# Performance work log

Measured on AMD Instinct MI355X. Metric: run time of the kernel, lower is better.

## Reference

```python
import jax, jax.numpy as jnp
import numpy as np

VOCAB, DM, H, DH, FF, NL = 50265, 768, 12, 64, 3072, 12
WIN = 256  # one-sided window (attention_window=512)
B, S = 1, 4096


def layer_norm(x, s, b, eps=1e-5):
    mu = x.mean(-1, keepdims=True)
    var = x.var(-1, keepdims=True)
    return (x - mu) * jax.lax.rsqrt(var + eps) * s + b


def sliding_attn(x, key_mask, wq, wk, wv, bq, bk, bv):
    Bb, Ss, _ = x.shape
    nb = Ss // WIN
    q = ((x @ wq + bq) / np.float32(np.sqrt(DH))).reshape(Bb, nb, WIN, H, DH)
    k = (x @ wk + bk).reshape(Bb, Ss, H, DH)
    v = (x @ wv + bv).reshape(Bb, Ss, H, DH)
    pad = [(0, 0), (WIN, WIN), (0, 0), (0, 0)]
    kp = jnp.pad(k, pad).reshape(Bb, nb + 2, WIN, H, DH)
    vp = jnp.pad(v, pad).reshape(Bb, nb + 2, WIN, H, DH)
    mp = jnp.pad(key_mask, [(0, 0), (WIN, WIN)]).reshape(Bb, nb + 2, WIN)
    kwin = jnp.concatenate([kp[:, i:i + nb] for i in range(3)], axis=2)  # [B,nb,3W,H,DH]
    vwin = jnp.concatenate([vp[:, i:i + nb] for i in range(3)], axis=2)
    mwin = jnp.concatenate([mp[:, i:i + nb] for i in range(3)], axis=2)  # [B,nb,3W]
    scores = jnp.einsum('bnqhd,bnkhd->bhnqk', q, kwin)  # [B,H,nb,W,3W]
    rel = jnp.arange(3 * WIN)[None, :] - jnp.arange(WIN)[:, None]
    band = (rel >= 0) & (rel <= 2 * WIN)
    valid = band[None, None, None] & (mwin > 0)[:, None, :, None, :]
    probs = jax.nn.softmax(jnp.where(valid, scores, -1e9), axis=-1)
    out = jnp.einsum('bhnqk,bnkhd->bnqhd', probs, vwin)
    return out.reshape(Bb, Ss, H * DH)


def encode(tokens, mask, word_emb, pos_emb, emb_ln_s, emb_ln_b, qkv_w, qkv_b,
           attn_out_w, attn_out_b, attn_ln_s, attn_ln_b,
           ffn_w1, ffn_b1, ffn_w2, ffn_b2, ffn_ln_s, ffn_ln_b):
    Ss = tokens.shape[1]
    x = word_emb[tokens] + pos_emb[2:2 + Ss][None]  # roberta-style position offset
    x = layer_norm(x, emb_ln_s, emb_ln_b)
    for l in range(NL):
        a = sliding_attn(x, mask, qkv_w[l, 0], qkv_w[l, 1], qkv_w[l, 2],
                         qkv_b[l, 0], qkv_b[l, 1], qkv_b[l, 2])
        x = layer_norm(x + a @ attn_out_w[l] + attn_out_b[l], attn_ln_s[l], attn_ln_b[l])
        h = jax.nn.gelu(x @ ffn_w1[l] + ffn_b1[l], approximate=False)
        x = layer_norm(x + h @ ffn_w2[l] + ffn_b2[l], ffn_ln_s[l], ffn_ln_b[l])
    return x


def setup_inputs() -> dict:
    key = jax.random.key(0)
    ks = iter(jax.random.split(key, 40))
    tokens = jax.random.randint(next(ks), (B, 1, S), 0, VOCAB)
    mask = jnp.ones((B, 1, S), dtype=jnp.int64 if False else jnp.int32)
    essay_tokens = jnp.concatenate([tokens, mask.astype(tokens.dtype)], axis=1)
    g = lambda shape: (jax.random.normal(next(ks), shape, jnp.float32) * 0.02)
    return {
        'essay_tokens': essay_tokens,
        'word_emb': g((VOCAB, DM)), 'pos_emb': g((4098, DM)),
        'emb_ln_s': jnp.ones((DM,)), 'emb_ln_b': jnp.zeros((DM,)),
        'qkv_w': g((NL, 3, DM, DM)), 'qkv_b': g((NL, 3, DM)),
        'attn_out_w': g((NL, DM, DM)), 'attn_out_b': g((NL, DM)),
        'attn_ln_s': jnp.ones((NL, DM)), 'attn_ln_b': jnp.zeros((NL, DM)),
        'ffn_w1': g((NL, DM, FF)), 'ffn_b1': g((NL, FF)),
        'ffn_w2': g((NL, FF, DM)), 'ffn_b2': g((NL, DM)),
        'ffn_ln_s': jnp.ones((NL, DM)), 'ffn_ln_b': jnp.zeros((NL, DM)),
        'cls_w1': g((DM, 512)), 'cls_b1': jnp.zeros((512,)),
        'cls_w2': g((512, 512)), 'cls_b2': jnp.zeros((512,)),
        'cls_w3': g((512, 512)), 'cls_b3': jnp.zeros((512,)),
        'cls_w4': g((512, 2)), 'cls_b4': jnp.zeros((2,)),
    }


def reference(essay_tokens, word_emb, pos_emb, emb_ln_s, emb_ln_b, qkv_w, qkv_b,
              attn_out_w, attn_out_b, attn_ln_s, attn_ln_b,
              ffn_w1, ffn_b1, ffn_w2, ffn_b2, ffn_ln_s, ffn_ln_b,
              cls_w1, cls_b1, cls_w2, cls_b2, cls_w3, cls_b3, cls_w4, cls_b4):
    tokens = essay_tokens[:, 0, :].astype(jnp.int32)
    mask = essay_tokens[:, 1, :].astype(jnp.int32)
    enc = encode(tokens, mask, word_emb, pos_emb, emb_ln_s, emb_ln_b, qkv_w, qkv_b,
                 attn_out_w, attn_out_b, attn_ln_s, attn_ln_b,
                 ffn_w1, ffn_b1, ffn_w2, ffn_b2, ffn_ln_s, ffn_ln_b)
    # torch.no_grad() on the transformer
    enc = jax.lax.stop_gradient(enc)
    h = enc @ cls_w1 + cls_b1
    h = h @ cls_w2 + cls_b2
    h = h @ cls_w3 + cls_b3
    logits = h @ cls_w4 + cls_b4  # [B,S,2]
    out = logits[..., 0]          # chunk(..., 2, dim=-1)[0] then flatten(1)
    return out.reshape(out.shape[0], -1)
```

## Files before the change

### kernel.cpp

```cpp
#include <hip/hip_runtime.h>
#include <cmath>

#define S_LEN 4096
#define DMODEL 768
#define NHEAD 12
#define DHEAD 64
#define FFDIM 3072
#define NLAYER 12
#define WINR 256

typedef float f32x4 __attribute__((ext_vector_type(4)));
typedef short s8v __attribute__((ext_vector_type(8)));
typedef __bf16 b8v __attribute__((ext_vector_type(8)));

__device__ __forceinline__ short f2b(float f) {
  unsigned u = __builtin_bit_cast(unsigned, f);
  unsigned r = (u + 0x7fffu + ((u >> 16) & 1u)) >> 16;
  return (short)r;
}
__device__ __forceinline__ float b2f(short s) {
  unsigned u = ((unsigned)(unsigned short)s) << 16;
  return __builtin_bit_cast(float, u);
}
__device__ __forceinline__ f32x4 mfma16(s8v a, s8v b, f32x4 c) {
  return __builtin_amdgcn_mfma_f32_16x16x32_bf16(
      __builtin_bit_cast(b8v, a), __builtin_bit_cast(b8v, b), c, 0, 0, 0);
}
__device__ __forceinline__ void gl_lds16(const short* g, short* l) {
  __builtin_amdgcn_global_load_lds(
      (const __attribute__((address_space(1))) unsigned int*)g,
      (__attribute__((address_space(3))) unsigned int*)l, 16, 0, 0);
}

#define QSCALE 0.18033688011112042f
#define THR2 11.5415603f

__device__ __forceinline__ void wtr_tile(const float* __restrict__ src,
                                         short* __restrict__ dst, int K, int N,
                                         int k0, int n0, int t,
                                         short (*tile)[65]) {
  {
    int kr = t >> 2, nc = (t & 3) * 16;
    const float* p = src + (long)(k0 + kr) * N + n0 + nc;
#pragma unroll
    for (int q = 0; q < 4; ++q) {
      float4 f = *(const float4*)(p + q * 4);
      tile[kr][nc + q * 4 + 0] = f2b(f.x);
      tile[kr][nc + q * 4 + 1] = f2b(f.y);
      tile[kr][nc + q * 4 + 2] = f2b(f.z);
      tile[kr][nc + q * 4 + 3] = f2b(f.w);
    }
  }
  __syncthreads();
  {
    int nr = t >> 2, cc = (t & 3) * 16;
    short* q = dst + (long)(n0 + nr) * K + k0 + cc;
    s8v v0, v1;
#pragma unroll
    for (int j = 0; j < 8; ++j) v0[j] = tile[cc + j][nr];
#pragma unroll
    for (int j = 0; j < 8; ++j) v1[j] = tile[cc + 8 + j][nr];
    *(s8v*)q = v0;
    *(s8v*)(q + 8) = v1;
  }
}

__global__ __launch_bounds__(256) void wtr_kernel(const float* __restrict__ src,
                                                  short* __restrict__ dst,
                                                  int K, int N) {
  __shared__ short tile[64][65];
  wtr_tile(src, dst, K, N, blockIdx.y * 64, blockIdx.x * 64, threadIdx.x, tile);
}

__global__ __launch_bounds__(256) void wtr_layer_kernel(
    const float* __restrict__ qkv, const float* __restrict__ ao,
    const float* __restrict__ w1, const float* __restrict__ w2,
    short* __restrict__ lwq, short* __restrict__ lwa, short* __restrict__ lw1,
    short* __restrict__ lw2) {
  __shared__ short tile[64][65];
  const long DD = (long)DMODEL * DMODEL;
  int id = blockIdx.x;
  const float* src;
  short* dst;
  int K, N, nT, kT;
  if (id < 432) {
    int m = id / 144, r = id % 144;
    src = qkv + m * DD; dst = lwq + m * DD;
    K = DMODEL; N = DMODEL; nT = r % 12; kT = r / 12;
  } else if (id < 576) {
    int r = id - 432;
    src = ao; dst = lwa;
    K = DMODEL; N = DMODEL; nT = r % 12; kT = r / 12;
  } else if (id < 1152) {
    int r = id - 576;
    src = w1; dst = lw1;
    K = DMODEL; N = FFDIM; nT = r % 48; kT = r / 48;
  } else {
    int r = id - 1152;
    src = w2; dst = lw2;
    K = FFDIM; N = DMODEL; nT = r % 12; kT = r / 12;
  }
  wtr_tile(src, dst, K, N, kT * 64, nT * 64, threadIdx.x, tile);
}

template <int EPI, int OUT>
__global__ __launch_bounds__(256, 4) void bgemm_kernel(
    const short* __restrict__ A, const short* __restrict__ Bt,
    const float* __restrict__ bias, void* __restrict__ Cv,
    int N, int K, int Klen, long sB, long sBias, long sC) {
  __shared__ short As[2][128 * 32];
  __shared__ short Bs[2][128 * 32];
  const int t = threadIdx.x, lane = t & 63, w = t >> 6;
  const int lo = lane & 15, hi = lane >> 4;
  const int wm = (w >> 1) * 64, wn = (w & 1) * 64;

  const int gx = gridDim.x;
  const int bid = blockIdx.x + gx * (blockIdx.y + 32 * blockIdx.z);
  const int xcd = bid & 7;
  const int jj_ = bid >> 3;
  const int bx = jj_ % gx;
  const int t2 = jj_ / gx;
  const int by = xcd * 4 + (t2 & 3);
  const int bz = t2 >> 2;

  const long bm = (long)by * 128;
  const int bn = bx * 128;
  Bt += (long)bz * sB;
  const long Koff = (OUT == 2) ? (long)bz * Klen : 0;

  f32x4 acc[4][4];
#pragma unroll
  for (int i = 0; i < 4; ++i)
#pragma unroll
    for (int j = 0; j < 4; ++j) {
      f32x4 zz = {0.f, 0.f, 0.f, 0.f};
      acc[i][j] = zz;
    }

  const int srow = lane >> 2;
  const int schunk = (lane & 3) ^ ((lane >> 3) & 3);
  const short* ga = A + (bm + srow) * (long)K + Koff + schunk * 8;
  const short* gb = Bt + ((long)bn + srow) * K + Koff + schunk * 8;

#define STAGE(buf, koff)                                                   \
  {                                                                        \
    _Pragma("unroll") for (int i = 0; i < 2; ++i) {                        \
      const int r0 = i * 64 + w * 16;                                      \
      gl_lds16(ga + (long)r0 * K + (koff), As[buf] + r0 * 32);             \
      gl_lds16(gb + (long)r0 * K + (koff), Bs[buf] + r0 * 32);             \
    }                                                                      \
  }

  STAGE(0, 0);
  __syncthreads();

  const int nt = Klen >> 5;
  const int rchunk = (hi ^ ((lo >> 1) & 3)) * 8;
  for (int kt = 0; kt < nt; ++kt) {
    const int cur = kt & 1;
    if (kt + 1 < nt) STAGE(cur ^ 1, (kt + 1) * 32);
    s8v af[4], bf[4];
#pragma unroll
    for (int mi = 0; mi < 4; ++mi)
      af[mi] = *(const s8v*)(As[cur] + (wm + mi * 16 + lo) * 32 + rchunk);
#pragma unroll
    for (int ni = 0; ni < 4; ++ni)
      bf[ni] = *(const s8v*)(Bs[cur] + (wn + ni * 16 + lo) * 32 + rchunk);
#pragma unroll
    for (int mi = 0; mi < 4; ++mi)
#pragma unroll
      for (int ni = 0; ni < 4; ++ni)
        acc[mi][ni] = mfma16(af[mi], bf[ni], acc[mi][ni]);
    __syncthreads();
  }
#undef STAGE

  const float sc = (EPI == 2 && bz == 0) ? QSCALE : 1.0f;
  float* Cf = (float*)Cv + (long)bz * sC;
  short* Cs = (short*)Cv + (long)bz * sC;
  const float* bp = bias + (long)bz * sBias;
#pragma unroll
  for (int mi = 0; mi < 4; ++mi)
#pragma unroll
    for (int ni = 0; ni < 4; ++ni) {
      int col = bn + wn + ni * 16 + lo;
      float bb = (OUT == 2) ? 0.f : bp[col];
#pragma unroll
      for (int jj = 0; jj < 4; ++jj) {
        long row = bm + wm + mi * 16 + hi * 4 + jj;
        float v = acc[mi][ni][jj] + bb;
        if (EPI == 2) v *= sc;
        if (EPI == 1) v = 0.5f * v * (1.0f + erff(v * 0.7071067811865476f));
        if (OUT == 1)
          Cs[row * N + col] = f2b(v);
        else
          Cf[row * N + col] = v;
      }
    }
}

__global__ __launch_bounds__(256) void attn_kernel(
    const short* __restrict__ Qb, const short* __restrict__ Kb,
    const short* __restrict__ Vb, const int* __restrict__ maskp,
    short* __restrict__ Ob) {
  __shared__ short Ks[2][64 * 64];
  __shared__ short VT[2][64 * 64];
  __shared__ short Pl[4][16 * 64];

  const int t = threadIdx.x, lane = t & 63, w = t >> 6;
  const int lo = lane & 15, hi = lane >> 4;

  const int bid = blockIdx.x + 64 * blockIdx.y;
  const int xcd = bid & 7, jb = bid >> 3;
  const int qb = xcd * 8 + (jb & 7), h = jb >> 3;

  const int q0 = qb * 64;
  const int qw = q0 + w * 16;
  short* Plw = Pl[w];

  s8v aq[2];
#pragma unroll
  for (int kg = 0; kg < 2; ++kg)
    aq[kg] = *(const s8v*)(Qb + (long)(qw + lo) * DMODEL + h * 64 + kg * 32 +
                           hi * 8);

  f32x4 o[4];
#pragma unroll
  for (int i = 0; i < 4; ++i) {
    f32x4 zz = {0.f, 0.f, 0.f, 0.f};
    o[i] = zz;
  }
  float rm[4], rl[4];
#pragma unroll
  for (int r = 0; r < 4; ++r) { rm[r] = -1e30f; rl[r] = 0.f; }

  const int kstart = max(0, q0 - WINR);
  const int kend = min(S_LEN, q0 + 64 + WINR);
  const int nt = (kend - kstart) >> 6;

  const int krow = lane >> 3;
  const int ksrccol = ((lane & 7) ^ krow) * 8;

  {
#pragma unroll
    for (int i = 0; i < 2; ++i) {
      const int r0 = w * 16 + i * 8;
      gl_lds16(Kb + (long)(kstart + r0 + krow) * DMODEL + h * 64 + ksrccol,
               Ks[0] + r0 * 64);
    }
    const short* pv = Vb + (long)(kstart + lane) * DMODEL + h * 64 + w * 16;
    s8v v0 = *(const s8v*)pv;
    s8v v1 = *(const s8v*)(pv + 8);
#pragma unroll
    for (int j = 0; j < 8; ++j)
      VT[0][(w * 16 + j) * 64 + (lane ^ (j << 3))] = v0[j];
#pragma unroll
    for (int j = 0; j < 8; ++j)
      VT[0][(w * 16 + 8 + j) * 64 + (lane ^ (j << 3))] = v1[j];
  }
  __syncthreads();

  for (int ti = 0; ti < nt; ++ti) {
    const int kt = kstart + ti * 64;
    const int cur = ti & 1;
    const bool pf = (ti + 1 < nt);
    s8v nv0, nv1;
    if (pf) {
#pragma unroll
      for (int i = 0; i < 2; ++i) {
        const int r0 = w * 16 + i * 8;
        gl_lds16(Kb + (long)(kt + 64 + r0 + krow) * DMODEL + h * 64 + ksrccol,
                 Ks[cur ^ 1] + r0 * 64);
      }
      const short* pv = Vb + (long)(kt + 64 + lane) * DMODEL + h * 64 + w * 16;
      nv0 = *(const s8v*)pv;
      nv1 = *(const s8v*)(pv + 8);
    }

    const bool active = (kt + 63 >= qw - WINR) && (kt <= qw + 15 + WINR);
    if (active) {
      f32x4 sacc[4];
#pragma unroll
      for (int i = 0; i < 4; ++i) {
        f32x4 zz = {0.f, 0.f, 0.f, 0.f};
        sacc[i] = zz;
      }
#pragma unroll
      for (int ni = 0; ni < 4; ++ni)
#pragma unroll
        for (int kg = 0; kg < 2; ++kg) {
          const int chunk = (kg * 4 + hi) ^ (lo & 7);
          s8v bk = *(const s8v*)(Ks[cur] + (ni * 16 + lo) * 64 + chunk * 8);
          sacc[ni] = mfma16(aq[kg], bk, sacc[ni]);
        }

      int mval[4];
#pragma unroll
      for (int ni = 0; ni < 4; ++ni) mval[ni] = maskp[kt + ni * 16 + lo];

      float m0[4];
#pragma unroll
      for (int jj = 0; jj < 4; ++jj) {
        const int qg = qw + hi * 4 + jj;
        float mm = -1e30f;
#pragma unroll
        for (int ni = 0; ni < 4; ++ni) {
          int kg = kt + ni * 16 + lo;
          bool val = (kg >= qg - WINR) && (kg <= qg + WINR) && (mval[ni] != 0);
          float sv = val ? sacc[ni][jj] : -1e30f;
          sacc[ni][jj] = sv;
          mm = fmaxf(mm, sv);
        }
        mm = fmaxf(mm, __shfl_xor(mm, 1));
        mm = fmaxf(mm, __shfl_xor(mm, 2));
        mm = fmaxf(mm, __shfl_xor(mm, 4));
        mm = fmaxf(mm, __shfl_xor(mm, 8));
        m0[jj] = mm;
      }

      bool skipf = true;
#pragma unroll
      for (int jj = 0; jj < 4; ++jj) skipf = skipf && (m0[jj] - rm[jj] <= THR2);

      if (__all(skipf)) {
#pragma unroll
        for (int jj = 0; jj < 4; ++jj) {
          float ts = 0.f;
#pragma unroll
          for (int ni = 0; ni < 4; ++ni) {
            float sv = sacc[ni][jj];
            float p = (sv > -1e29f) ? exp2f(sv - rm[jj]) : 0.f;
            sacc[ni][jj] = p;
            ts += p;
          }
          ts += __shfl_xor(ts, 1);
          ts += __shfl_xor(ts, 2);
          ts += __shfl_xor(ts, 4);
          ts += __shfl_xor(ts, 8);
          rl[jj] += ts;
        }
      } else {
#pragma unroll
        for (int jj = 0; jj < 4; ++jj) {
          float mnew = fmaxf(rm[jj], m0[jj]);
          float scl = exp2f(rm[jj] - mnew);
          rm[jj] = mnew;
          float ts = 0.f;
#pragma unroll
          for (int ni = 0; ni < 4; ++ni) {
            float sv = sacc[ni][jj];
            float p = (sv > -1e29f) ? exp2f(sv - mnew) : 0.f;
            sacc[ni][jj] = p;
            ts += p;
          }
          ts += __shfl_xor(ts, 1);
          ts += __shfl_xor(ts, 2);
          ts += __shfl_xor(ts, 4);
          ts += __shfl_xor(ts, 8);
          rl[jj] = rl[jj] * scl + ts;
#pragma unroll
          for (int di = 0; di < 4; ++di) o[di][jj] *= scl;
        }
      }

#pragma unroll
      for (int jj = 0; jj < 4; ++jj) {
        const int qr = hi * 4 + jj;
#pragma unroll
        for (int ni = 0; ni < 4; ++ni) {
          const int chunk = (ni * 2 + (lo >> 3)) ^ (qr & 7);
          Plw[qr * 64 + chunk * 8 + (lo & 7)] = f2b(sacc[ni][jj]);
        }
      }

      s8v ap[2];
#pragma unroll
      for (int kg = 0; kg < 2; ++kg) {
        const int chunk = (kg * 4 + hi) ^ (lo & 7);
        ap[kg] = *(const s8v*)(Plw + lo * 64 + chunk * 8);
      }
#pragma unroll
      for (int di = 0; di < 4; ++di)
#pragma unroll
        for (int kg = 0; kg < 2; ++kg) {
          const int chunk = (kg * 4 + hi) ^ (lo & 7);
          s8v bv = *(const s8v*)(VT[cur] + (di * 16 + lo) * 64 + chunk * 8);
          o[di] = mfma16(ap[kg], bv, o[di]);
        }
    }

    if (pf) {
#pragma unroll
      for (int j = 0; j < 8; ++j)
        VT[cur ^ 1][(w * 16 + j) * 64 + (lane ^ (j << 3))] = nv0[j];
#pragma unroll
      for (int j = 0; j < 8; ++j)
        VT[cur ^ 1][(w * 16 + 8 + j) * 64 + (lane ^ (j << 3))] = nv1[j];
    }
    __syncthreads();
  }

#pragma unroll
  for (int di = 0; di < 4; ++di)
#pragma unroll
    for (int jj = 0; jj < 4; ++jj) {
      long row = qw + hi * 4 + jj;
      Ob[row * DMODEL + h * 64 + di * 16 + lo] = f2b(o[di][jj] / rl[jj]);
    }
}

__global__ __launch_bounds__(256) void embed_ln_kernel(
    const int* __restrict__ tok, const float* __restrict__ wemb,
    const float* __restrict__ pemb, const float* __restrict__ gs,
    const float* __restrict__ gb, float* __restrict__ X,
    short* __restrict__ Xb) {
  __shared__ float sm1[4], sm2[4];
  const int row = blockIdx.x;
  const int tk = tok[row];
  float v[3];
  float s = 0.f, q = 0.f;
#pragma unroll
  for (int i = 0; i < 3; ++i) {
    int c = threadIdx.x + i * 256;
    float x = wemb[(long)tk * DMODEL + c] + pemb[(long)(row + 2) * DMODEL + c];
    v[i] = x;
    s += x;
    q += x * x;
  }
#pragma unroll
  for (int off = 32; off; off >>= 1) {
    s += __shfl_down(s, off);
    q += __shfl_down(q, off);
  }
  int w = threadIdx.x >> 6;
  if ((threadIdx.x & 63) == 0) { sm1[w] = s; sm2[w] = q; }
  __syncthreads();
  s = sm1[0] + sm1[1] + sm1[2] + sm1[3];
  q = sm2[0] + sm2[1] + sm2[2] + sm2[3];
  float mu = s * (1.f / DMODEL);
  float var = q * (1.f / DMODEL) - mu * mu;
  float inv = rsqrtf(var + 1e-5f);
#pragma unroll
  for (int i = 0; i < 3; ++i) {
    int c = threadIdx.x + i * 256;
    float y = (v[i] - mu) * inv * gs[c] + gb[c];
    X[(long)row * DMODEL + c] = y;
    Xb[(long)row * DMODEL + c] = f2b(y);
  }
}

__global__ __launch_bounds__(256) void resln2_kernel(
    float* __restrict__ X, const float* __restrict__ P0,
    const float* __restrict__ P1, const float* __restrict__ bias,
    const float* __restrict__ gs, const float* __restrict__ gb,
    short* __restrict__ Xb) {
  __shared__ float sm1[4], sm2[4];
  const int row = blockIdx.x;
  float v[3];
  float s = 0.f, q = 0.f;
#pragma unroll
  for (int i = 0; i < 3; ++i) {
    int c = threadIdx.x + i * 256;
    long ix = (long)row * DMODEL + c;
    float x = X[ix] + P0[ix] + P1[ix] + bias[c];
    v[i] = x;
    s += x;
    q += x * x;
  }
#pragma unroll
  for (int off = 32; off; off >>= 1) {
    s += __shfl_down(s, off);
    q += __shfl_down(q, off);
  }
  int w = threadIdx.x >> 6;
  if ((threadIdx.x & 63) == 0) { sm1[w] = s; sm2[w] = q; }
  __syncthreads();
  s = sm1[0] + sm1[1] + sm1[2] + sm1[3];
  q = sm2[0] + sm2[1] + sm2[2] + sm2[3];
  float mu = s * (1.f / DMODEL);
  float var = q * (1.f / DMODEL) - mu * mu;
  float inv = rsqrtf(var + 1e-5f);
#pragma unroll
  for (int i = 0; i < 3; ++i) {
    int c = threadIdx.x + i * 256;
    float y = (v[i] - mu) * inv * gs[c] + gb[c];
    X[(long)row * DMODEL + c] = y;
    Xb[(long)row * DMODEL + c] = f2b(y);
  }
}

__global__ __launch_bounds__(256) void cls_final_kernel(
    const short* __restrict__ Hh, const float* __restrict__ w4,
    const float* __restrict__ b4, float* __restrict__ out) {
  const int w = threadIdx.x >> 6, lane = threadIdx.x & 63;
  const int row = blockIdx.x * 4 + w;
  float s = 0.f;
#pragma unroll
  for (int j = 0; j < 8; ++j) {
    int k = lane + j * 64;
    s += b2f(Hh[(long)row * 512 + k]) * w4[k * 2];
  }
#pragma unroll
  for (int off = 32; off; off >>= 1) s += __shfl_down(s, off);
  if (lane == 0) out[row] = s + b4[0];
}

extern "C" void kernel_launch(void* const* d_in, const int* in_sizes, int n_in,
                              void* d_out, int out_size, void* d_ws,
                              size_t ws_size, hipStream_t stream) {
  const int* essay = (const int*)d_in[0];
  const float* wemb = (const float*)d_in[1];
  const float* pemb = (const float*)d_in[2];
  const float* eln_s = (const float*)d_in[3];
  const float* eln_b = (const float*)d_in[4];
  const float* qkv_w = (const float*)d_in[5];
  const float* qkv_b = (const float*)d_in[6];
  const float* aow = (const float*)d_in[7];
  const float* aob = (const float*)d_in[8];
  const float* aln_s = (const float*)d_in[9];
  const float* aln_b = (const float*)d_in[10];
  const float* w1 = (const float*)d_in[11];
  const float* b1 = (const float*)d_in[12];
  const float* w2 = (const float*)d_in[13];
  const float* b2 = (const float*)d_in[14];
  const float* fln_s = (const float*)d_in[15];
  const float* fln_b = (const float*)d_in[16];
  const float* c1w = (const float*)d_in[17];
  const float* c1b = (const float*)d_in[18];
  const float* c2w = (const float*)d_in[19];
  const float* c2b = (const float*)d_in[20];
  const float* c3w = (const float*)d_in[21];
  const float* c3b = (const float*)d_in[22];
  const float* c4w = (const float*)d_in[23];
  const float* c4b = (const float*)d_in[24];

  const long SD = (long)S_LEN * DMODEL;
  const long SF = (long)S_LEN * FFDIM;
  const long SH = (long)S_LEN * 512;
  const long DD = (long)DMODEL * DMODEL;
  const long DF = (long)DMODEL * FFDIM;

  float* X = (float*)d_ws;
  float* P0 = X + SD;
  float* P1 = P0 + SD;
  short* lwq = (short*)(P1 + SD);
  short* lwa = lwq + 3 * DD;
  short* lw1 = lwa + DD;
  short* lw2 = lw1 + DF;
  short* c1T = lw2 + DF;
  short* c2T = c1T + (long)DMODEL * 512;
  short* c3T = c2T + 512L * 512;
  short* Xb = c3T + 512L * 512;
  short* QKVb = Xb + SD;
  short* T1b = QKVb + 3 * SD;
  short* T2b = T1b + SD;
  short* H1 = T2b + SF;
  short* H2 = H1 + SH;
  short* H3 = H2 + SH;
  const long needed = (char*)(H3 + SH) - (char*)d_ws;
  if (ws_size < (size_t)needed) return;

  const int* maskp = essay + S_LEN;

  embed_ln_kernel<<<S_LEN, 256, 0, stream>>>(essay, wemb, pemb, eln_s, eln_b, X,
                                             Xb);

  for (int l = 0; l < NLAYER; ++l) {
    wtr_layer_kernel<<<1728, 256, 0, stream>>>(
        qkv_w + l * 3 * DD, aow + l * DD, w1 + l * DF, w2 + l * DF, lwq, lwa,
        lw1, lw2);

    bgemm_kernel<2, 1><<<dim3(6, 32, 3), 256, 0, stream>>>(
        Xb, lwq, qkv_b + (long)l * 3 * DMODEL, QKVb, DMODEL, DMODEL, DMODEL, DD,
        DMODEL, SD);
    attn_kernel<<<dim3(64, 12), 256, 0, stream>>>(QKVb, QKVb + SD,
                                                  QKVb + 2 * SD, maskp, T1b);
    bgemm_kernel<0, 2><<<dim3(6, 32, 2), 256, 0, stream>>>(
        T1b, lwa, aob, P0, DMODEL, DMODEL, 384, 0, 0, SD);
    resln2_kernel<<<S_LEN, 256, 0, stream>>>(X, P0, P1, aob + (long)l * DMODEL,
                                             aln_s + (long)l * DMODEL,
                                             aln_b + (long)l * DMODEL, Xb);
    bgemm_kernel<1, 1><<<dim3(24, 32, 1), 256, 0, stream>>>(
        Xb, lw1, b1 + (long)l * FFDIM, T2b, FFDIM, DMODEL, DMODEL, 0, 0, 0);
    bgemm_kernel<0, 2><<<dim3(6, 32, 2), 256, 0, stream>>>(
        T2b, lw2, b2, P0, DMODEL, FFDIM, 1536, 0, 0, SD);
    resln2_kernel<<<S_LEN, 256, 0, stream>>>(X, P0, P1, b2 + (long)l * DMODEL,
                                             fln_s + (long)l * DMODEL,
                                             fln_b + (long)l * DMODEL, Xb);
  }

  wtr_kernel<<<dim3(8, 12), 256, 0, stream>>>(c1w, c1T, DMODEL, 512);
  wtr_kernel<<<dim3(8, 8), 256, 0, stream>>>(c2w, c2T, 512, 512);
  wtr_kernel<<<dim3(8, 8), 256, 0, stream>>>(c3w, c3T, 512, 512);

  bgemm_kernel<0, 1><<<dim3(4, 32, 1), 256, 0, stream>>>(
      Xb, c1T, c1b, H1, 512, DMODEL, DMODEL, 0, 0, 0);
  bgemm_kernel<0, 1><<<dim3(4, 32, 1), 256, 0, stream>>>(H1, c2T, c2b, H2, 512,
                                                         512, 512, 0, 0, 0);
  bgemm_kernel<0, 1><<<dim3(4, 32, 1), 256, 0, stream>>>(H2, c3T, c3b, H3, 512,
                                                         512, 512, 0, 0, 0);
  cls_final_kernel<<<S_LEN / 4, 256, 0, stream>>>(H3, c4w, c4b, (float*)d_out);
}
```

Measured before the change: 2.343 ms.

## Pre-transpose V globally, async-stage K/V tiles, store split-K partials in bf16

Adds a separate kernel that transposes V into a head-major [dim, seq] layout, so the attention kernel can stage both K and V tiles with async global-to-LDS loads instead of register loads followed by scattered LDS stores. It also adds a fast masking path for key tiles that lie fully inside the window. The split-K GEMM partial outputs become bf16 instead of fp32, roughly halving the traffic into the residual-layernorm kernel. The costs are an extra kernel launch per layer and lower precision on the partial sums before layernorm.

```diff
diff --git a/kernel.cpp b/kernel.cpp
--- a/kernel.cpp
+++ b/kernel.cpp
@@ -103,6 +103,35 @@
   wtr_tile(src, dst, K, N, kT * 64, nT * 64, threadIdx.x, tile);
 }
 
+__global__ __launch_bounds__(256) void vtr_kernel(const short* __restrict__ Vb,
+                                                  short* __restrict__ VTg) {
+  __shared__ short tile[64][65];
+  const int s0 = blockIdx.x * 64, h = blockIdx.y;
+  const int t = threadIdx.x;
+  {
+    int sr = t >> 2, dc = (t & 3) * 16;
+    const short* p = Vb + (long)(s0 + sr) * DMODEL + h * 64 + dc;
+    s8v a0 = *(const s8v*)p;
+    s8v a1 = *(const s8v*)(p + 8);
+#pragma unroll
+    for (int j = 0; j < 8; ++j) tile[sr][dc + j] = a0[j];
+#pragma unroll
+    for (int j = 0; j < 8; ++j) tile[sr][dc + 8 + j] = a1[j];
+  }
+  __syncthreads();
+  {
+    int dr = t >> 2, sc = (t & 3) * 16;
+    short* q = VTg + (long)(h * 64 + dr) * S_LEN + s0 + sc;
+    s8v v0, v1;
+#pragma unroll
+    for (int j = 0; j < 8; ++j) v0[j] = tile[sc + j][dr];
+#pragma unroll
+    for (int j = 0; j < 8; ++j) v1[j] = tile[sc + 8 + j][dr];
+    *(s8v*)q = v0;
+    *(s8v*)(q + 8) = v1;
+  }
+}
+
 template <int EPI, int OUT>
 __global__ __launch_bounds__(256, 4) void bgemm_kernel(
     const short* __restrict__ A, const short* __restrict__ Bt,
@@ -191,17 +220,17 @@
         float v = acc[mi][ni][jj] + bb;
         if (EPI == 2) v *= sc;
         if (EPI == 1) v = 0.5f * v * (1.0f + erff(v * 0.7071067811865476f));
-        if (OUT == 1)
+        if (OUT == 0)
+          Cf[row * N + col] = v;
+        else
           Cs[row * N + col] = f2b(v);
-        else
-          Cf[row * N + col] = v;
       }
     }
 }
 
 __global__ __launch_bounds__(256) void attn_kernel(
     const short* __restrict__ Qb, const short* __restrict__ Kb,
-    const short* __restrict__ Vb, const int* __restrict__ maskp,
+    const short* __restrict__ VTg, const int* __restrict__ maskp,
     short* __restrict__ Ob) {
   __shared__ short Ks[2][64 * 64];
   __shared__ short VT[2][64 * 64];
@@ -239,43 +268,27 @@
   const int nt = (kend - kstart) >> 6;
 
   const int krow = lane >> 3;
-  const int ksrccol = ((lane & 7) ^ krow) * 8;
-
-  {
-#pragma unroll
-    for (int i = 0; i < 2; ++i) {
-      const int r0 = w * 16 + i * 8;
-      gl_lds16(Kb + (long)(kstart + r0 + krow) * DMODEL + h * 64 + ksrccol,
-               Ks[0] + r0 * 64);
-    }
-    const short* pv = Vb + (long)(kstart + lane) * DMODEL + h * 64 + w * 16;
-    s8v v0 = *(const s8v*)pv;
-    s8v v1 = *(const s8v*)(pv + 8);
-#pragma unroll
-    for (int j = 0; j < 8; ++j)
-      VT[0][(w * 16 + j) * 64 + (lane ^ (j << 3))] = v0[j];
-#pragma unroll
-    for (int j = 0; j < 8; ++j)
-      VT[0][(w * 16 + 8 + j) * 64 + (lane ^ (j << 3))] = v1[j];
-  }
+  const int kxor = ((lane & 7) ^ krow) * 8;
+  const long vrow = (long)(h * 64 + w * 16 + krow) * S_LEN;
+
+#define STAGE_KV(buf, kt)                                                    \
+  {                                                                          \
+    _Pragma("unroll") for (int i = 0; i < 2; ++i) {                          \
+      const int r0 = w * 16 + i * 8;                                         \
+      gl_lds16(Kb + (long)((kt) + r0 + krow) * DMODEL + h * 64 + kxor,       \
+               Ks[buf] + r0 * 64);                                           \
+      gl_lds16(VTg + vrow + (long)i * 8 * S_LEN + (kt) + kxor,               \
+               VT[buf] + r0 * 64);                                           \
+    }                                                                        \
+  }
+
+  STAGE_KV(0, kstart);
   __syncthreads();
 
   for (int ti = 0; ti < nt; ++ti) {
     const int kt = kstart + ti * 64;
     const int cur = ti & 1;
-    const bool pf = (ti + 1 < nt);
-    s8v nv0, nv1;
-    if (pf) {
-#pragma unroll
-      for (int i = 0; i < 2; ++i) {
-        const int r0 = w * 16 + i * 8;
-        gl_lds16(Kb + (long)(kt + 64 + r0 + krow) * DMODEL + h * 64 + ksrccol,
-                 Ks[cur ^ 1] + r0 * 64);
-      }
-      const short* pv = Vb + (long)(kt + 64 + lane) * DMODEL + h * 64 + w * 16;
-      nv0 = *(const s8v*)pv;
-      nv1 = *(const s8v*)(pv + 8);
-    }
+    if (ti + 1 < nt) STAGE_KV(cur ^ 1, kt + 64);
 
     const bool active = (kt + 63 >= qw - WINR) && (kt <= qw + 15 + WINR);
     if (active) {
@@ -298,24 +311,44 @@
 #pragma unroll
       for (int ni = 0; ni < 4; ++ni) mval[ni] = maskp[kt + ni * 16 + lo];
 
+      const bool fullband = (kt >= qw + 15 - WINR) && (kt + 63 <= qw + WINR);
+
       float m0[4];
-#pragma unroll
-      for (int jj = 0; jj < 4; ++jj) {
-        const int qg = qw + hi * 4 + jj;
-        float mm = -1e30f;
-#pragma unroll
-        for (int ni = 0; ni < 4; ++ni) {
-          int kg = kt + ni * 16 + lo;
-          bool val = (kg >= qg - WINR) && (kg <= qg + WINR) && (mval[ni] != 0);
-          float sv = val ? sacc[ni][jj] : -1e30f;
-          sacc[ni][jj] = sv;
-          mm = fmaxf(mm, sv);
+      if (fullband) {
+#pragma unroll
+        for (int jj = 0; jj < 4; ++jj) {
+          float mm = -1e30f;
+#pragma unroll
+          for (int ni = 0; ni < 4; ++ni) {
+            float sv = (mval[ni] != 0) ? sacc[ni][jj] : -1e30f;
+            sacc[ni][jj] = sv;
+            mm = fmaxf(mm, sv);
+          }
+          mm = fmaxf(mm, __shfl_xor(mm, 1));
+          mm = fmaxf(mm, __shfl_xor(mm, 2));
+          mm = fmaxf(mm, __shfl_xor(mm, 4));
+          mm = fmaxf(mm, __shfl_xor(mm, 8));
+          m0[jj] = mm;
         }
-        mm = fmaxf(mm, __shfl_xor(mm, 1));
-        mm = fmaxf(mm, __shfl_xor(mm, 2));
-        mm = fmaxf(mm, __shfl_xor(mm, 4));
-        mm = fmaxf(mm, __shfl_xor(mm, 8));
-        m0[jj] = mm;
+      } else {
+#pragma unroll
+        for (int jj = 0; jj < 4; ++jj) {
+          const int qg = qw + hi * 4 + jj;
+          float mm = -1e30f;
+#pragma unroll
+          for (int ni = 0; ni < 4; ++ni) {
+            int kg = kt + ni * 16 + lo;
+            bool val = (kg >= qg - WINR) && (kg <= qg + WINR) && (mval[ni] != 0);
+            float sv = val ? sacc[ni][jj] : -1e30f;
+            sacc[ni][jj] = sv;
+            mm = fmaxf(mm, sv);
+          }
+          mm = fmaxf(mm, __shfl_xor(mm, 1));
+          mm = fmaxf(mm, __shfl_xor(mm, 2));
+          mm = fmaxf(mm, __shfl_xor(mm, 4));
+          mm = fmaxf(mm, __shfl_xor(mm, 8));
+          m0[jj] = mm;
+        }
       }
 
       bool skipf = true;
@@ -388,17 +421,9 @@
           o[di] = mfma16(ap[kg], bv, o[di]);
         }
     }
-
-    if (pf) {
-#pragma unroll
-      for (int j = 0; j < 8; ++j)
-        VT[cur ^ 1][(w * 16 + j) * 64 + (lane ^ (j << 3))] = nv0[j];
-#pragma unroll
-      for (int j = 0; j < 8; ++j)
-        VT[cur ^ 1][(w * 16 + 8 + j) * 64 + (lane ^ (j << 3))] = nv1[j];
-    }
     __syncthreads();
   }
+#undef STAGE_KV
 
 #pragma unroll
   for (int di = 0; di < 4; ++di)
@@ -450,8 +475,8 @@
 }
 
 __global__ __launch_bounds__(256) void resln2_kernel(
-    float* __restrict__ X, const float* __restrict__ P0,
-    const float* __restrict__ P1, const float* __restrict__ bias,
+    float* __restrict__ X, const short* __restrict__ P0b,
+    const short* __restrict__ P1b, const float* __restrict__ bias,
     const float* __restrict__ gs, const float* __restrict__ gb,
     short* __restrict__ Xb) {
   __shared__ float sm1[4], sm2[4];
@@ -462,7 +487,7 @@
   for (int i = 0; i < 3; ++i) {
     int c = threadIdx.x + i * 256;
     long ix = (long)row * DMODEL + c;
-    float x = X[ix] + P0[ix] + P1[ix] + bias[c];
+    float x = X[ix] + b2f(P0b[ix]) + b2f(P1b[ix]) + bias[c];
     v[i] = x;
     s += x;
     q += x * x;
@@ -543,6 +568,9 @@
   float* X = (float*)d_ws;
   float* P0 = X + SD;
   float* P1 = P0 + SD;
+  short* P0b = (short*)P0;
+  short* P1b = P0b + SD;
+  short* VTg = (short*)P1;
   short* lwq = (short*)(P1 + SD);
   short* lwa = lwq + 3 * DD;
   short* lw1 = lwa + DD;
@@ -573,18 +601,21 @@
     bgemm_kernel<2, 1><<<dim3(6, 32, 3), 256, 0, stream>>>(
         Xb, lwq, qkv_b + (long)l * 3 * DMODEL, QKVb, DMODEL, DMODEL, DMODEL, DD,
         DMODEL, SD);
-    attn_kernel<<<dim3(64, 12), 256, 0, stream>>>(QKVb, QKVb + SD,
-                                                  QKVb + 2 * SD, maskp, T1b);
+    vtr_kernel<<<dim3(64, 12), 256, 0, stream>>>(QKVb + 2 * SD, VTg);
+    attn_kernel<<<dim3(64, 12), 256, 0, stream>>>(QKVb, QKVb + SD, VTg, maskp,
+                                                  T1b);
     bgemm_kernel<0, 2><<<dim3(6, 32, 2), 256, 0, stream>>>(
-        T1b, lwa, aob, P0, DMODEL, DMODEL, 384, 0, 0, SD);
-    resln2_kernel<<<S_LEN, 256, 0, stream>>>(X, P0, P1, aob + (long)l * DMODEL,
+        T1b, lwa, aob, P0b, DMODEL, DMODEL, 384, 0, 0, SD);
+    resln2_kernel<<<S_LEN, 256, 0, stream>>>(X, P0b, P1b,
+                                             aob + (long)l * DMODEL,
                                              aln_s + (long)l * DMODEL,
                                              aln_b + (long)l * DMODEL, Xb);
     bgemm_kernel<1, 1><<<dim3(24, 32, 1), 256, 0, stream>>>(
         Xb, lw1, b1 + (long)l * FFDIM, T2b, FFDIM, DMODEL, DMODEL, 0, 0, 0);
     bgemm_kernel<0, 2><<<dim3(6, 32, 2), 256, 0, stream>>>(
-        T2b, lw2, b2, P0, DMODEL, FFDIM, 1536, 0, 0, SD);
-    resln2_kernel<<<S_LEN, 256, 0, stream>>>(X, P0, P1, b2 + (long)l * DMODEL,
+        T2b, lw2, b2, P0b, DMODEL, FFDIM, 1536, 0, 0, SD);
+    resln2_kernel<<<S_LEN, 256, 0, stream>>>(X, P0b, P1b,
+                                             b2 + (long)l * DMODEL,
                                              fln_s + (long)l * DMODEL,
                                              fln_b + (long)l * DMODEL, Xb);
   }
```

Measured after the change: 2.247 ms. 4.1% less time.
